# Kernel optimization log

Measured on AMD Instinct MI355X. Metric: run time of the kernel, lower is better.

## Reference

```python
import jax, jax.numpy as jnp
import numpy as np

P = 3           # planes (u, v, y)
N = 50000       # nodes per plane
E = 256000      # edges per plane
C = 5           # num_classes
F_IN, F_NODE, F_EDGE = 4, 64, 16
F = F_IN + F_NODE  # 68, per-node feature dim


def setup_inputs() -> dict:
    key = jax.random.key(0)
    ks = jax.random.split(key, 10)
    s = 0.05  # weight scale for numerical sanity
    return {
        "x": jax.random.normal(ks[0], (P, N, C, F), jnp.float32),
        "edge_index": jax.random.randint(ks[1], (P, 2, E), 0, N, dtype=jnp.int64),
        "We1": jax.random.normal(ks[2], (P, C, F_EDGE, 2 * F), jnp.float32) * s,
        "be1": jax.random.normal(ks[3], (P, C, F_EDGE), jnp.float32) * s,
        "We2": jax.random.normal(ks[4], (P, C, 1, F_EDGE), jnp.float32) * s,
        "be2": jax.random.normal(ks[5], (P, C, 1), jnp.float32) * s,
        "Wn1": jax.random.normal(ks[6], (P, C, F_NODE, 2 * F), jnp.float32) * s,
        "bn1": jax.random.normal(ks[7], (P, C, F_NODE), jnp.float32) * s,
        "Wn2": jax.random.normal(ks[8], (P, C, F_NODE, F_NODE), jnp.float32) * s,
        "bn2": jax.random.normal(ks[9], (P, C, F_NODE), jnp.float32) * s,
    }


def class_linear(x, W, b):
    # x: [n, C, fin], W: [C, fout, fin], b: [C, fout] -> [n, C, fout]
    return jnp.einsum('ncf,cgf->ncg', x, W) + b


def mp_plane(x, ei, We1, be1, We2, be2, Wn1, bn1, Wn2, bn2):
    # MessagePassing2D (source_to_target): x_j = source, x_i = target
    src, dst = ei[0], ei[1]
    x_i = x[dst]                                # [E, C, F]
    x_j = x[src]                                # [E, C, F]
    # edge_net input is detached in the original (stop_gradient)
    m_in = jax.lax.stop_gradient(jnp.concatenate([x_i, x_j], axis=-1))  # [E, C, 2F]
    h = jnp.tanh(class_linear(m_in, We1, be1))  # [E, C, F_EDGE]
    logits = class_linear(h, We2, be2)          # [E, C, 1]
    w = jax.nn.softmax(logits, axis=1)          # softmax over class dim (dim=1)
    msg = w * x_j                               # [E, C, F]
    aggr = jax.ops.segment_sum(msg, dst, num_segments=N)  # scatter-add to targets
    u_in = jnp.concatenate([x, aggr], axis=-1)  # [N, C, 2F]
    h2 = jnp.tanh(class_linear(u_in, Wn1, bn1))
    return jnp.tanh(class_linear(h2, Wn2, bn2))  # [N, C, F_NODE]


def reference(x, edge_index, We1, be1, We2, be2, Wn1, bn1, Wn2, bn2):
    # vmap over the 3 detector planes (PlaneNet ModuleDict)
    return jax.vmap(mp_plane)(x, edge_index, We1, be1, We2, be2,
                              Wn1, bn1, Wn2, bn2)  # [P, N, C, F_NODE]
```

## Files before the change

### kernel.cpp

```cpp
#include <hip/hip_runtime.h>
#include <hip/hip_fp16.h>
#include <math.h>

constexpr int kP  = 3;
constexpr int kN  = 50000;
constexpr int kE  = 256000;
constexpr int kC  = 5;
constexpr int kF  = 68;
constexpr int kF2 = 136;
constexpr int kFE = 16;
constexpr int kFN = 64;
constexpr int kOfsStride = 50004;
constexpr int kNChunks = (kN + 1023) / 1024;
constexpr int kPartStride = 64;

__device__ __forceinline__ float fast_tanh(float x) {
  float t = fminf(fmaxf(x, -15.f), 15.f);
  float e = __expf(2.f * t);
  return (e - 1.f) / (e + 1.f);
}

__global__ __launch_bounds__(256) void hist_kernel(
    const int* __restrict__ ei,
    int* __restrict__ counts)
{
  int p = blockIdx.y;
  int e = blockIdx.x * 256 + threadIdx.x;
  if (e >= kE) return;
  int dst = ei[(size_t)p * 2 * kE + kE + e];
  atomicAdd(&counts[p * kN + dst], 1);
}

__global__ __launch_bounds__(256) void scanA_kernel(
    const int* __restrict__ counts,
    int* __restrict__ offsets,
    int* __restrict__ partials)
{
  int p = blockIdx.y, chunk = blockIdx.x, tid = threadIdx.x;
  const int* cnt = counts + p * kN;
  int base = chunk * 1024 + tid * 4;
  int v0 = 0, v1 = 0, v2 = 0, v3 = 0;
  if (base + 3 < kN) {
    int4 v = *reinterpret_cast<const int4*>(cnt + base);
    v0 = v.x; v1 = v.y; v2 = v.z; v3 = v.w;
  } else if (base < kN) {
    v0 = cnt[base];
    if (base + 1 < kN) v1 = cnt[base + 1];
    if (base + 2 < kN) v2 = cnt[base + 2];
  }
  int s0 = v0, s1 = s0 + v1, s2 = s1 + v2, s3 = s2 + v3;
  __shared__ int buf[256];
  buf[tid] = s3;
  __syncthreads();
  for (int d = 1; d < 256; d <<= 1) {
    int t = (tid >= d) ? buf[tid - d] : 0;
    __syncthreads();
    buf[tid] += t;
    __syncthreads();
  }
  int excl = buf[tid] - s3;
  int* ofs = offsets + p * kOfsStride;
  if (base + 3 < kN) {
    *reinterpret_cast<int4*>(ofs + base) =
        make_int4(excl, excl + s0, excl + s1, excl + s2);
  } else if (base < kN) {
    ofs[base] = excl;
    if (base + 1 < kN) ofs[base + 1] = excl + s0;
    if (base + 2 < kN) ofs[base + 2] = excl + s1;
  }
  if (tid == 255) partials[p * kPartStride + chunk] = buf[255];
}

__global__ __launch_bounds__(64) void scanB_kernel(int* __restrict__ partials)
{
  int p = blockIdx.x, tid = threadIdx.x;
  int v = (tid < kNChunks) ? partials[p * kPartStride + tid] : 0;
  __shared__ int buf[64];
  buf[tid] = v;
  __syncthreads();
  for (int d = 1; d < 64; d <<= 1) {
    int t = (tid >= d) ? buf[tid - d] : 0;
    __syncthreads();
    buf[tid] += t;
    __syncthreads();
  }
  partials[p * kPartStride + tid] = buf[tid] - v;
}

__global__ __launch_bounds__(256) void scanC_kernel(
    int* __restrict__ offsets,
    const int* __restrict__ partials,
    int* __restrict__ cursor)
{
  int p = blockIdx.y, chunk = blockIdx.x, tid = threadIdx.x;
  int add = partials[p * kPartStride + chunk];
  int base = chunk * 1024 + tid * 4;
  int* ofs = offsets + p * kOfsStride;
  int* cur = cursor + p * kN;
  if (base + 3 < kN) {
    int4 v = *reinterpret_cast<const int4*>(ofs + base);
    v.x += add; v.y += add; v.z += add; v.w += add;
    *reinterpret_cast<int4*>(ofs + base) = v;
    *reinterpret_cast<int4*>(cur + base) = v;
  } else if (base < kN) {
#pragma unroll
    for (int k = 0; k < 3; ++k) {
      if (base + k < kN) {
        int o = ofs[base + k] + add;
        ofs[base + k] = o;
        cur[base + k] = o;
      }
    }
  }
  if (chunk == 0 && tid == 0) ofs[kN] = partials[p * kPartStride + kNChunks];
}

__global__ __launch_bounds__(256) void pre_kernel(
    const float* __restrict__ x,
    const float* __restrict__ We1,
    float* __restrict__ yi,
    float* __restrict__ yj)
{
  int n = blockIdx.x * 256 + threadIdx.x;
  int c = blockIdx.y;
  if (n >= kN) return;

  const float4* xr = reinterpret_cast<const float4*>(x + ((size_t)n * kC + c) * kF);
  const float* Wc = We1 + c * (kFE * kF2);

  float ai[kFE], aj[kFE];
#pragma unroll
  for (int g = 0; g < kFE; ++g) { ai[g] = 0.f; aj[g] = 0.f; }

  for (int q = 0; q < kF / 4; ++q) {
    float4 v = xr[q];
#pragma unroll
    for (int g = 0; g < kFE; ++g) {
      const float* wi = Wc + g * kF2 + 4 * q;
      const float* wj = wi + kF;
      float a = ai[g];
      a = fmaf(wi[0], v.x, a); a = fmaf(wi[1], v.y, a);
      a = fmaf(wi[2], v.z, a); a = fmaf(wi[3], v.w, a);
      ai[g] = a;
      float b = aj[g];
      b = fmaf(wj[0], v.x, b); b = fmaf(wj[1], v.y, b);
      b = fmaf(wj[2], v.z, b); b = fmaf(wj[3], v.w, b);
      aj[g] = b;
    }
  }

  float4* oi = reinterpret_cast<float4*>(yi + ((size_t)n * kC + c) * kFE);
  float4* oj = reinterpret_cast<float4*>(yj + ((size_t)n * kC + c) * kFE);
#pragma unroll
  for (int k = 0; k < 4; ++k) {
    oi[k] = make_float4(ai[4*k], ai[4*k+1], ai[4*k+2], ai[4*k+3]);
    oj[k] = make_float4(aj[4*k], aj[4*k+1], aj[4*k+2], aj[4*k+3]);
  }
}

__global__ __launch_bounds__(256) void pre_z_kernel(
    const float* __restrict__ x,
    const float* __restrict__ Wn1,
    __half* __restrict__ z)
{
  int n = blockIdx.x * 256 + threadIdx.x;
  int c = blockIdx.y;
  if (n >= kN) return;

  float4 xr[kF / 4];
  const float4* xp = reinterpret_cast<const float4*>(x + ((size_t)n * kC + c) * kF);
#pragma unroll
  for (int q = 0; q < kF / 4; ++q) xr[q] = xp[q];

  const float* W = Wn1 + c * (kFN * kF2) + kF;
  uint4* zp = reinterpret_cast<uint4*>(z + ((size_t)n * kC + c) * kFN);

  for (int g0 = 0; g0 < kFN; g0 += 8) {
    float acc[8];
#pragma unroll
    for (int t = 0; t < 8; ++t) acc[t] = 0.f;
#pragma unroll
    for (int q = 0; q < kF / 4; ++q) {
      float4 v = xr[q];
#pragma unroll
      for (int t = 0; t < 8; ++t) {
        const float* wr = W + (size_t)(g0 + t) * kF2 + 4 * q;
        float a = acc[t];
        a = fmaf(wr[0], v.x, a); a = fmaf(wr[1], v.y, a);
        a = fmaf(wr[2], v.z, a); a = fmaf(wr[3], v.w, a);
        acc[t] = a;
      }
    }
    __half2 p0 = __floats2half2_rn(acc[0], acc[1]);
    __half2 p1 = __floats2half2_rn(acc[2], acc[3]);
    __half2 p2 = __floats2half2_rn(acc[4], acc[5]);
    __half2 p3 = __floats2half2_rn(acc[6], acc[7]);
    uint4 pk;
    pk.x = *reinterpret_cast<unsigned int*>(&p0);
    pk.y = *reinterpret_cast<unsigned int*>(&p1);
    pk.z = *reinterpret_cast<unsigned int*>(&p2);
    pk.w = *reinterpret_cast<unsigned int*>(&p3);
    zp[g0 >> 3] = pk;
  }
}

__global__ __launch_bounds__(256) void edge_kernel(
    const int*   __restrict__ ei,
    const float* __restrict__ yi,
    const float* __restrict__ yj,
    const float* __restrict__ be1,
    const float* __restrict__ We2,
    const float* __restrict__ be2,
    int*         __restrict__ cursor,
    int*         __restrict__ sorted_src,
    float*       __restrict__ w_sorted)
{
  int e = blockIdx.x * 256 + threadIdx.x;
  if (e >= kE) return;
  int src = ei[e];
  int dst = ei[kE + e];

  const float* yid = yi + (size_t)dst * (kC * kFE);
  const float* yjs = yj + (size_t)src * (kC * kFE);

  float logits[kC];
#pragma unroll
  for (int c = 0; c < kC; ++c) {
    const float4* a = reinterpret_cast<const float4*>(yid + c * kFE);
    const float4* b = reinterpret_cast<const float4*>(yjs + c * kFE);
    float lg = be2[c];
#pragma unroll
    for (int qq = 0; qq < 4; ++qq) {
      float4 av = a[qq];
      float4 bv = b[qq];
      const float* bb = be1 + c * kFE + 4 * qq;
      const float* w2 = We2 + c * kFE + 4 * qq;
      lg = fmaf(w2[0], fast_tanh(av.x + bv.x + bb[0]), lg);
      lg = fmaf(w2[1], fast_tanh(av.y + bv.y + bb[1]), lg);
      lg = fmaf(w2[2], fast_tanh(av.z + bv.z + bb[2]), lg);
      lg = fmaf(w2[3], fast_tanh(av.w + bv.w + bb[3]), lg);
    }
    logits[c] = lg;
  }

  float m = logits[0];
#pragma unroll
  for (int c = 1; c < kC; ++c) m = fmaxf(m, logits[c]);
  float wgt[kC];
  float s = 0.f;
#pragma unroll
  for (int c = 0; c < kC; ++c) { wgt[c] = __expf(logits[c] - m); s += wgt[c]; }
  float inv = 1.f / s;

  int pos = atomicAdd(&cursor[dst], 1);
  sorted_src[pos] = src;
#pragma unroll
  for (int c = 0; c < kC; ++c) w_sorted[(size_t)pos * kC + c] = wgt[c] * inv;
}

__global__ __launch_bounds__(256) void node_split_kernel(
    const float*  __restrict__ x,
    const int*    __restrict__ offsets,
    const int*    __restrict__ sorted_src,
    const float*  __restrict__ w_sorted,
    const __half* __restrict__ z,
    const float*  __restrict__ Wn1,
    const float*  __restrict__ bn1,
    const float*  __restrict__ Wn2,
    const float*  __restrict__ bn2,
    float*        __restrict__ out)
{
  int i = blockIdx.x * 256 + threadIdx.x;
  int n = i >> 1;
  int half = i & 1;
  int c = blockIdx.y;
  if (n >= kN) return;

  int beg = offsets[n];
  int end = offsets[n + 1];
  int deg = end - beg;
  int hcnt = (deg + 1) >> 1;
  int s0 = beg + half * hcnt;
  int s1 = half ? end : beg + hcnt;

  float h[kFN];
#pragma unroll
  for (int g = 0; g < kFN; ++g) h[g] = 0.f;

  for (int s = s0; s < s1; ++s) {
    int sj = sorted_src[s];
    float w = w_sorted[(size_t)s * kC + c];
    const uint4* zp = reinterpret_cast<const uint4*>(
        z + ((size_t)sj * kC + c) * kFN);
#pragma unroll
    for (int u = 0; u < 8; ++u) {
      uint4 v = zp[u];
      float2 f0 = __half22float2(*reinterpret_cast<const __half2*>(&v.x));
      float2 f1 = __half22float2(*reinterpret_cast<const __half2*>(&v.y));
      float2 f2 = __half22float2(*reinterpret_cast<const __half2*>(&v.z));
      float2 f3 = __half22float2(*reinterpret_cast<const __half2*>(&v.w));
      h[8*u+0] = fmaf(w, f0.x, h[8*u+0]);
      h[8*u+1] = fmaf(w, f0.y, h[8*u+1]);
      h[8*u+2] = fmaf(w, f1.x, h[8*u+2]);
      h[8*u+3] = fmaf(w, f1.y, h[8*u+3]);
      h[8*u+4] = fmaf(w, f2.x, h[8*u+4]);
      h[8*u+5] = fmaf(w, f2.y, h[8*u+5]);
      h[8*u+6] = fmaf(w, f3.x, h[8*u+6]);
      h[8*u+7] = fmaf(w, f3.y, h[8*u+7]);
    }
  }

#pragma unroll
  for (int g = 0; g < kFN; ++g) h[g] += __shfl_xor(h[g], 1);

  const float* W1 = Wn1 + c * (kFN * kF2);
  const float4* xp = reinterpret_cast<const float4*>(x + ((size_t)n * kC + c) * kF);
  for (int q = 0; q < kF / 4; ++q) {
    float4 v = xp[q];
#pragma unroll
    for (int g = 0; g < kFN; ++g) {
      const float* wr = W1 + (size_t)g * kF2 + 4 * q;
      float a = h[g];
      a = fmaf(wr[0], v.x, a);
      a = fmaf(wr[1], v.y, a);
      a = fmaf(wr[2], v.z, a);
      a = fmaf(wr[3], v.w, a);
      h[g] = a;
    }
  }

  const float* b1 = bn1 + c * kFN;
#pragma unroll
  for (int g = 0; g < kFN; ++g) h[g] = fast_tanh(h[g] + b1[g]);

  const float* W2 = Wn2 + c * (kFN * kFN);
  const float* b2 = bn2 + c * kFN;
  float* op = out + ((size_t)n * kC + c) * kFN;
  for (int g2 = 0; g2 < kFN; g2 += 4) {
    float a0 = b2[g2], a1 = b2[g2 + 1], a2 = b2[g2 + 2], a3 = b2[g2 + 3];
    const float* w0 = W2 + (size_t)g2 * kFN;
#pragma unroll
    for (int k = 0; k < kFN; ++k) {
      float hk = h[k];
      a0 = fmaf(w0[k],            hk, a0);
      a1 = fmaf(w0[kFN + k],      hk, a1);
      a2 = fmaf(w0[2 * kFN + k],  hk, a2);
      a3 = fmaf(w0[3 * kFN + k],  hk, a3);
    }
    if ((g2 >> 5) == half) {
      *reinterpret_cast<float4*>(op + g2) =
          make_float4(fast_tanh(a0), fast_tanh(a1),
                      fast_tanh(a2), fast_tanh(a3));
    }
  }
}

extern "C" void kernel_launch(void* const* d_in, const int* in_sizes, int n_in,
                              void* d_out, int out_size, void* d_ws, size_t ws_size,
                              hipStream_t stream) {
  const float* x   = (const float*)d_in[0];
  const int*   ei  = (const int*)  d_in[1];
  const float* We1 = (const float*)d_in[2];
  const float* be1 = (const float*)d_in[3];
  const float* We2 = (const float*)d_in[4];
  const float* be2 = (const float*)d_in[5];
  const float* Wn1 = (const float*)d_in[6];
  const float* bn1 = (const float*)d_in[7];
  const float* Wn2 = (const float*)d_in[8];
  const float* bn2 = (const float*)d_in[9];
  float* out = (float*)d_out;

  int* counts  = (int*)d_ws;
  int* offsets = counts + kP * kN;
  int* cursor  = offsets + kP * kOfsStride;
  int* partials = cursor + kP * kN;
  int* sorted_src = partials + kP * kPartStride;
  float* w_sorted = (float*)(sorted_src + kE);
  float* yi = w_sorted + (size_t)kE * kC;
  float* yj = yi + (size_t)kN * kC * kFE;
  __half* z = (__half*)yi;

  const size_t planeX = (size_t)kN * kC * kF;

  hipMemsetAsync(counts, 0, (size_t)kP * kN * sizeof(int), stream);
  hist_kernel<<<dim3(kE / 256, kP), 256, 0, stream>>>(ei, counts);
  scanA_kernel<<<dim3(kNChunks, kP), 256, 0, stream>>>(counts, offsets, partials);
  scanB_kernel<<<kP, 64, 0, stream>>>(partials);
  scanC_kernel<<<dim3(kNChunks, kP), 256, 0, stream>>>(offsets, partials, cursor);

  for (int p = 0; p < kP; ++p) {
    const float* xp = x + p * planeX;

    pre_kernel<<<dim3((kN + 255) / 256, kC), 256, 0, stream>>>(
        xp, We1 + (size_t)p * kC * kFE * kF2, yi, yj);

    edge_kernel<<<kE / 256, 256, 0, stream>>>(
        ei + (size_t)p * 2 * kE, yi, yj,
        be1 + (size_t)p * kC * kFE,
        We2 + (size_t)p * kC * kFE,
        be2 + (size_t)p * kC,
        cursor + p * kN, sorted_src, w_sorted);

    pre_z_kernel<<<dim3((kN + 255) / 256, kC), 256, 0, stream>>>(
        xp, Wn1 + (size_t)p * kC * kFN * kF2, z);

    node_split_kernel<<<dim3((2 * kN + 255) / 256, kC), 256, 0, stream>>>(
        xp, offsets + p * kOfsStride, sorted_src, w_sorted, z,
        Wn1 + (size_t)p * kC * kFN * kF2,
        bn1 + (size_t)p * kC * kFN,
        Wn2 + (size_t)p * kC * kFN * kFN,
        bn2 + (size_t)p * kC * kFN,
        out + (size_t)p * kN * kC * kFN);
  }
}
```

Measured before the change: 2.120 ms.

## Precompute node x-projection and split node update across four lanes

Moves the x-part of the first node linear layer, plus its bias, into the pre-node kernel. That kernel writes the pre-activation into the output buffer as scratch. The node kernel now uses four lanes per node: two split the edge range and two split the feature halves. Lanes exchange halves via shuffles for the second linear layer, so each lane computes only 16 outputs. This removes the redundant full GEMVs that both half-threads previously did and cuts register pressure, at the cost of an extra write and read of a node-sized intermediate.

```diff
diff --git a/kernel.cpp b/kernel.cpp
--- a/kernel.cpp
+++ b/kernel.cpp
@@ -158,10 +158,12 @@
   }
 }
 
-__global__ __launch_bounds__(256) void pre_z_kernel(
+__global__ __launch_bounds__(256) void pre_node_kernel(
     const float* __restrict__ x,
     const float* __restrict__ Wn1,
-    __half* __restrict__ z)
+    const float* __restrict__ bn1,
+    __half* __restrict__ z,
+    float* hpre)
 {
   int n = blockIdx.x * 256 + threadIdx.x;
   int c = blockIdx.y;
@@ -172,9 +174,8 @@
 #pragma unroll
   for (int q = 0; q < kF / 4; ++q) xr[q] = xp[q];
 
-  const float* W = Wn1 + c * (kFN * kF2) + kF;
+  const float* Wz = Wn1 + c * (kFN * kF2) + kF;
   uint4* zp = reinterpret_cast<uint4*>(z + ((size_t)n * kC + c) * kFN);
-
   for (int g0 = 0; g0 < kFN; g0 += 8) {
     float acc[8];
 #pragma unroll
@@ -184,7 +185,7 @@
       float4 v = xr[q];
 #pragma unroll
       for (int t = 0; t < 8; ++t) {
-        const float* wr = W + (size_t)(g0 + t) * kF2 + 4 * q;
+        const float* wr = Wz + (size_t)(g0 + t) * kF2 + 4 * q;
         float a = acc[t];
         a = fmaf(wr[0], v.x, a); a = fmaf(wr[1], v.y, a);
         a = fmaf(wr[2], v.z, a); a = fmaf(wr[3], v.w, a);
@@ -202,6 +203,29 @@
     pk.w = *reinterpret_cast<unsigned int*>(&p3);
     zp[g0 >> 3] = pk;
   }
+
+  const float* Wx = Wn1 + c * (kFN * kF2);
+  const float* b1 = bn1 + c * kFN;
+  float4* hp = reinterpret_cast<float4*>(hpre + ((size_t)n * kC + c) * kFN);
+  for (int g0 = 0; g0 < kFN; g0 += 8) {
+    float acc[8];
+#pragma unroll
+    for (int t = 0; t < 8; ++t) acc[t] = b1[g0 + t];
+#pragma unroll
+    for (int q = 0; q < kF / 4; ++q) {
+      float4 v = xr[q];
+#pragma unroll
+      for (int t = 0; t < 8; ++t) {
+        const float* wr = Wx + (size_t)(g0 + t) * kF2 + 4 * q;
+        float a = acc[t];
+        a = fmaf(wr[0], v.x, a); a = fmaf(wr[1], v.y, a);
+        a = fmaf(wr[2], v.z, a); a = fmaf(wr[3], v.w, a);
+        acc[t] = a;
+      }
+    }
+    hp[(g0 >> 2)]     = make_float4(acc[0], acc[1], acc[2], acc[3]);
+    hp[(g0 >> 2) + 1] = make_float4(acc[4], acc[5], acc[6], acc[7]);
+  }
 }
 
 __global__ __launch_bounds__(256) void edge_kernel(
@@ -258,42 +282,41 @@
   for (int c = 0; c < kC; ++c) w_sorted[(size_t)pos * kC + c] = wgt[c] * inv;
 }
 
-__global__ __launch_bounds__(256) void node_split_kernel(
-    const float*  __restrict__ x,
+__global__ __launch_bounds__(256) void node_quad_kernel(
     const int*    __restrict__ offsets,
     const int*    __restrict__ sorted_src,
     const float*  __restrict__ w_sorted,
     const __half* __restrict__ z,
-    const float*  __restrict__ Wn1,
-    const float*  __restrict__ bn1,
     const float*  __restrict__ Wn2,
     const float*  __restrict__ bn2,
-    float*        __restrict__ out)
+    float*        out)
 {
   int i = blockIdx.x * 256 + threadIdx.x;
-  int n = i >> 1;
-  int half = i & 1;
+  int n = i >> 2;
+  if (n >= kN) return;
+  int q  = i & 3;
+  int eh = q & 1;
+  int hh = q >> 1;
   int c = blockIdx.y;
-  if (n >= kN) return;
 
   int beg = offsets[n];
   int end = offsets[n + 1];
   int deg = end - beg;
   int hcnt = (deg + 1) >> 1;
-  int s0 = beg + half * hcnt;
-  int s1 = half ? end : beg + hcnt;
-
-  float h[kFN];
-#pragma unroll
-  for (int g = 0; g < kFN; ++g) h[g] = 0.f;
+  int s0 = beg + eh * hcnt;
+  int s1 = eh ? end : beg + hcnt;
+
+  float h[32];
+#pragma unroll
+  for (int g = 0; g < 32; ++g) h[g] = 0.f;
 
   for (int s = s0; s < s1; ++s) {
     int sj = sorted_src[s];
     float w = w_sorted[(size_t)s * kC + c];
     const uint4* zp = reinterpret_cast<const uint4*>(
-        z + ((size_t)sj * kC + c) * kFN);
-#pragma unroll
-    for (int u = 0; u < 8; ++u) {
+        z + ((size_t)sj * kC + c) * kFN + hh * 32);
+#pragma unroll
+    for (int u = 0; u < 4; ++u) {
       uint4 v = zp[u];
       float2 f0 = __half22float2(*reinterpret_cast<const __half2*>(&v.x));
       float2 f1 = __half22float2(*reinterpret_cast<const __half2*>(&v.y));
@@ -311,48 +334,57 @@
   }
 
 #pragma unroll
-  for (int g = 0; g < kFN; ++g) h[g] += __shfl_xor(h[g], 1);
-
-  const float* W1 = Wn1 + c * (kFN * kF2);
-  const float4* xp = reinterpret_cast<const float4*>(x + ((size_t)n * kC + c) * kF);
-  for (int q = 0; q < kF / 4; ++q) {
-    float4 v = xp[q];
-#pragma unroll
-    for (int g = 0; g < kFN; ++g) {
-      const float* wr = W1 + (size_t)g * kF2 + 4 * q;
-      float a = h[g];
-      a = fmaf(wr[0], v.x, a);
-      a = fmaf(wr[1], v.y, a);
-      a = fmaf(wr[2], v.z, a);
-      a = fmaf(wr[3], v.w, a);
-      h[g] = a;
-    }
-  }
-
-  const float* b1 = bn1 + c * kFN;
-#pragma unroll
-  for (int g = 0; g < kFN; ++g) h[g] = fast_tanh(h[g] + b1[g]);
+  for (int g = 0; g < 32; ++g) h[g] += __shfl_xor(h[g], 1);
+
+  const float4* hp = reinterpret_cast<const float4*>(
+      out + ((size_t)n * kC + c) * kFN + hh * 32);
+#pragma unroll
+  for (int u = 0; u < 8; ++u) {
+    float4 v = hp[u];
+    h[4*u+0] = fast_tanh(h[4*u+0] + v.x);
+    h[4*u+1] = fast_tanh(h[4*u+1] + v.y);
+    h[4*u+2] = fast_tanh(h[4*u+2] + v.z);
+    h[4*u+3] = fast_tanh(h[4*u+3] + v.w);
+  }
 
   const float* W2 = Wn2 + c * (kFN * kFN);
   const float* b2 = bn2 + c * kFN;
-  float* op = out + ((size_t)n * kC + c) * kFN;
-  for (int g2 = 0; g2 < kFN; g2 += 4) {
-    float a0 = b2[g2], a1 = b2[g2 + 1], a2 = b2[g2 + 2], a3 = b2[g2 + 3];
-    const float* w0 = W2 + (size_t)g2 * kFN;
-#pragma unroll
-    for (int k = 0; k < kFN; ++k) {
-      float hk = h[k];
-      a0 = fmaf(w0[k],            hk, a0);
-      a1 = fmaf(w0[kFN + k],      hk, a1);
-      a2 = fmaf(w0[2 * kFN + k],  hk, a2);
-      a3 = fmaf(w0[3 * kFN + k],  hk, a3);
-    }
-    if ((g2 >> 5) == half) {
-      *reinterpret_cast<float4*>(op + g2) =
-          make_float4(fast_tanh(a0), fast_tanh(a1),
-                      fast_tanh(a2), fast_tanh(a3));
-    }
-  }
+  int g2base = q * 16;
+  int ofs_own = 32 * hh;
+  int ofs_oth = 32 - 32 * hh;
+
+  float acc[16];
+#pragma unroll
+  for (int j = 0; j < 16; ++j) acc[j] = b2[g2base + j];
+
+  for (int jc = 0; jc < 8; ++jc) {
+    float oth[4];
+#pragma unroll
+    for (int t = 0; t < 4; ++t) oth[t] = __shfl_xor(h[jc * 4 + t], 2);
+#pragma unroll
+    for (int j = 0; j < 16; ++j) {
+      const float* wr = W2 + (size_t)(g2base + j) * kFN;
+      float4 wo = *reinterpret_cast<const float4*>(wr + ofs_own + jc * 4);
+      float4 wt = *reinterpret_cast<const float4*>(wr + ofs_oth + jc * 4);
+      float a = acc[j];
+      a = fmaf(wo.x, h[jc*4+0], a);
+      a = fmaf(wo.y, h[jc*4+1], a);
+      a = fmaf(wo.z, h[jc*4+2], a);
+      a = fmaf(wo.w, h[jc*4+3], a);
+      a = fmaf(wt.x, oth[0], a);
+      a = fmaf(wt.y, oth[1], a);
+      a = fmaf(wt.z, oth[2], a);
+      a = fmaf(wt.w, oth[3], a);
+      acc[j] = a;
+    }
+  }
+
+  float* op = out + ((size_t)n * kC + c) * kFN + g2base;
+  float4* o4 = reinterpret_cast<float4*>(op);
+#pragma unroll
+  for (int u = 0; u < 4; ++u)
+    o4[u] = make_float4(fast_tanh(acc[4*u]),   fast_tanh(acc[4*u+1]),
+                        fast_tanh(acc[4*u+2]), fast_tanh(acc[4*u+3]));
 }
 
 extern "C" void kernel_launch(void* const* d_in, const int* in_sizes, int n_in,
@@ -381,6 +413,7 @@
   __half* z = (__half*)yi;
 
   const size_t planeX = (size_t)kN * kC * kF;
+  const size_t planeO = (size_t)kN * kC * kFN;
 
   hipMemsetAsync(counts, 0, (size_t)kP * kN * sizeof(int), stream);
   hist_kernel<<<dim3(kE / 256, kP), 256, 0, stream>>>(ei, counts);
@@ -390,6 +423,7 @@
 
   for (int p = 0; p < kP; ++p) {
     const float* xp = x + p * planeX;
+    float* outp = out + p * planeO;
 
     pre_kernel<<<dim3((kN + 255) / 256, kC), 256, 0, stream>>>(
         xp, We1 + (size_t)p * kC * kFE * kF2, yi, yj);
@@ -401,15 +435,14 @@
         be2 + (size_t)p * kC,
         cursor + p * kN, sorted_src, w_sorted);
 
-    pre_z_kernel<<<dim3((kN + 255) / 256, kC), 256, 0, stream>>>(
-        xp, Wn1 + (size_t)p * kC * kFN * kF2, z);
-
-    node_split_kernel<<<dim3((2 * kN + 255) / 256, kC), 256, 0, stream>>>(
-        xp, offsets + p * kOfsStride, sorted_src, w_sorted, z,
-        Wn1 + (size_t)p * kC * kFN * kF2,
-        bn1 + (size_t)p * kC * kFN,
+    pre_node_kernel<<<dim3((kN + 255) / 256, kC), 256, 0, stream>>>(
+        xp, Wn1 + (size_t)p * kC * kFN * kF2,
+        bn1 + (size_t)p * kC * kFN, z, outp);
+
+    node_quad_kernel<<<dim3((4 * kN + 255) / 256, kC), 256, 0, stream>>>(
+        offsets + p * kOfsStride, sorted_src, w_sorted, z,
         Wn2 + (size_t)p * kC * kFN * kFN,
         bn2 + (size_t)p * kC * kFN,
-        out + (size_t)p * kN * kC * kFN);
-  }
-}
+        outp);
+  }
+}
```

Result: slower. 3.034 ms (+43.1%).
